# Kernel tuning notes

Measured on AMD Instinct MI355X. Metric: run time of the kernel, lower is better.

The kernel has to match this reference:

```python
import jax, jax.numpy as jnp
import numpy as np

N, C, E = 100000, 128, 600000
H = C // 2  # 64


def setup_inputs() -> dict:
    key = jax.random.key(0)
    k1, k2, k3, k4, k5, k6, k7, k8 = jax.random.split(key, 8)
    z_in = jax.random.normal(k1, (N, C), dtype=jnp.float32)
    z_out = jax.random.normal(k2, (N, C), dtype=jnp.float32)
    z_self = jax.random.normal(k3, (N, C), dtype=jnp.float32)
    edge_index = jax.random.randint(k4, (2, E), 0, N, dtype=jnp.int64)
    # MLP params: Linear(C, C//2) -> ELU -> (Dropout eval=no-op) -> Linear(C//2, 1)
    lim1 = 1.0 / np.sqrt(C)
    W1 = jax.random.uniform(k5, (C, H), minval=-lim1, maxval=lim1, dtype=jnp.float32)
    b1 = jax.random.uniform(k6, (H,), minval=-lim1, maxval=lim1, dtype=jnp.float32)
    lim2 = 1.0 / np.sqrt(H)
    W2 = jax.random.uniform(k7, (H, 1), minval=-lim2, maxval=lim2, dtype=jnp.float32)
    b2 = jax.random.uniform(k8, (1,), minval=-lim2, maxval=lim2, dtype=jnp.float32)
    return {"z_in": z_in, "z_out": z_out, "z_self": z_self,
            "edge_index": edge_index, "W1": W1, "b1": b1, "W2": W2, "b2": b2}


def reference(z_in, z_out, z_self, edge_index, W1, b1, W2, b2):
    v1 = z_out + z_self                       # [N, C]
    v2 = z_in + z_self                        # [N, C]
    value = v1[edge_index[0]] * v2[edge_index[1]]  # [E, C] gather + elementwise product
    h = jax.nn.elu(value @ W1 + b1)           # [E, H]; dropout is identity at eval
    logits = h @ W2 + b2                      # [E, 1]
    return jax.nn.sigmoid(logits)
```

## Files before the change

kernel.cpp:

```cpp
#include <hip/hip_runtime.h>
#include <hip/hip_bf16.h>

typedef __attribute__((ext_vector_type(8))) short short8;
typedef __attribute__((ext_vector_type(4))) float f32x4;

__device__ __forceinline__ unsigned short f2bf(float f) {
    unsigned u = __float_as_uint(f);
    u += 0x7fffu + ((u >> 16) & 1u);
    return (unsigned short)(u >> 16);
}

__device__ __forceinline__ unsigned pack_trunc(float lo, float hi) {
    return __builtin_amdgcn_perm(__float_as_uint(hi), __float_as_uint(lo), 0x07060302u);
}


__global__ __launch_bounds__(256) void prep_i8(
    const f32x4* __restrict__ zin, const f32x4* __restrict__ zout,
    const f32x4* __restrict__ zself,
    unsigned* __restrict__ q1, unsigned* __restrict__ q2,
    float* __restrict__ s1, float* __restrict__ s2, int N)
{
    const int lane = threadIdx.x & 63;
    const int wave = threadIdx.x >> 6;
    const int h    = lane >> 5;
    const int l32  = lane & 31;
    const int row  = blockIdx.x * 8 + wave * 2 + h;
    if (row >= N) return;
    const size_t rb = (size_t)row * 32 + l32;

    f32x4 o = __builtin_nontemporal_load(zout  + rb);
    f32x4 s = __builtin_nontemporal_load(zself + rb);
    f32x4 z = __builtin_nontemporal_load(zin   + rb);
    float v1[4] = {o.x + s.x, o.y + s.y, o.z + s.z, o.w + s.w};
    float v2[4] = {z.x + s.x, z.y + s.y, z.z + s.z, z.w + s.w};

    float m1 = fmaxf(fmaxf(fabsf(v1[0]), fabsf(v1[1])),
                     fmaxf(fabsf(v1[2]), fabsf(v1[3])));
    float m2 = fmaxf(fmaxf(fabsf(v2[0]), fabsf(v2[1])),
                     fmaxf(fabsf(v2[2]), fabsf(v2[3])));
#pragma unroll
    for (int off = 1; off < 32; off <<= 1) {
        m1 = fmaxf(m1, __shfl_xor(m1, off, 64));
        m2 = fmaxf(m2, __shfl_xor(m2, off, 64));
    }
    m1 = fmaxf(m1, 1e-20f);
    m2 = fmaxf(m2, 1e-20f);
    const float i1 = 127.0f / m1, i2 = 127.0f / m2;

    int qa[4], qb[4];
#pragma unroll
    for (int j = 0; j < 4; j++) {
        qa[j] = (int)rintf(v1[j] * i1);
        qb[j] = (int)rintf(v2[j] * i2);
    }
    unsigned wa = (unsigned)(qa[0] & 255) | ((unsigned)(qa[1] & 255) << 8) |
                  ((unsigned)(qa[2] & 255) << 16) | ((unsigned)qa[3] << 24);
    unsigned wb = (unsigned)(qb[0] & 255) | ((unsigned)(qb[1] & 255) << 8) |
                  ((unsigned)(qb[2] & 255) << 16) | ((unsigned)qb[3] << 24);
    q1[rb] = wa; q2[rb] = wb;
    if (l32 == 0) {
        s1[row] = m1 * (1.0f / 127.0f);
        s2[row] = m2 * (1.0f / 127.0f);
    }
}

__device__ __forceinline__ float pmul(unsigned aw, unsigned bw, int sh) {
    int a = (int)(signed char)(aw >> sh);
    int b = (int)(signed char)(bw >> sh);
    return (float)(a * b);
}

__global__ __launch_bounds__(256, 4) void edge_pipe_i8(
    const unsigned* __restrict__ q1, const unsigned* __restrict__ q2,
    const float* __restrict__ s1, const float* __restrict__ s2,
    const int* __restrict__ idx,
    const float* __restrict__ W1, const float* __restrict__ b1,
    const float* __restrict__ W2, const float* __restrict__ b2,
    float* __restrict__ out, int E, int ntiles)
{
    __shared__ __align__(16) unsigned short ldsW[16 * 64 * 8];

    const int tid  = threadIdx.x;
    const int wave = tid >> 6;
    const int lane = tid & 63;
    const int nn = lane & 15;
    const int q  = lane >> 4;

#pragma unroll
    for (int i = 0; i < 4; i++) {
        int p = tid * 4 + i;
        int f = p >> 6, l = p & 63;
        int kc = f >> 2, jt = f & 3, lq = (l >> 4) & 3, ln = l & 15;
        const float* wp = W1 + (size_t)(kc * 32 + lq * 8) * 64 + jt * 16 + ln;
        uint4 wv;
        wv.x = (unsigned)f2bf(wp[0 * 64]) | ((unsigned)f2bf(wp[1 * 64]) << 16);
        wv.y = (unsigned)f2bf(wp[2 * 64]) | ((unsigned)f2bf(wp[3 * 64]) << 16);
        wv.z = (unsigned)f2bf(wp[4 * 64]) | ((unsigned)f2bf(wp[5 * 64]) << 16);
        wv.w = (unsigned)f2bf(wp[6 * 64]) | ((unsigned)f2bf(wp[7 * 64]) << 16);
        *(uint4*)&ldsW[p * 8] = wv;
    }
    __syncthreads();

    float bias1[4], w2v[4];
#pragma unroll
    for (int jt = 0; jt < 4; jt++) {
        bias1[jt] = b1[jt * 16 + nn];
        w2v[jt]   = W2[jt * 16 + nn];
    }
    const float b2v = b2[0];

    const int nwaves = gridDim.x * 4;
    int tile = blockIdx.x * 4 + wave;
    if (tile >= ntiles) return;
    const int* __restrict__ idxE = idx + E;

    const int e0  = min(tile * 16 + nn, E - 1);
    const int t1  = tile + nwaves;
    const int tc1 = (t1 < ntiles) ? t1 : tile;
    const int e1  = min(tc1 * 16 + nn, E - 1);
    const int src0 = __builtin_nontemporal_load(idx  + e0);
    const int dst0 = __builtin_nontemporal_load(idxE + e0);
    int srcn = __builtin_nontemporal_load(idx  + e1);
    int dstn = __builtin_nontemporal_load(idxE + e1);

    float sN_a = s1[src0], sN_b = s2[dst0];

    uint2 a[4], b[4];
    {
        const uint2* p1 = (const uint2*)q1 + (size_t)src0 * 16;
        const uint2* p2 = (const uint2*)q2 + (size_t)dst0 * 16;
#pragma unroll
        for (int kc = 0; kc < 4; kc++) { a[kc] = p1[kc * 4 + q]; b[kc] = p2[kc * 4 + q]; }
    }

    for (; tile < ntiles; tile += nwaves) {
        const int t2  = tile + 2 * nwaves;
        const int tc2 = (t2 < ntiles) ? t2 : tile;
        const int e2  = min(tc2 * 16 + nn, E - 1);
        const int src2 = __builtin_nontemporal_load(idx  + e2);
        const int dst2 = __builtin_nontemporal_load(idxE + e2);

        const float s12 = sN_a * sN_b;
        short8 Af[4];
#pragma unroll
        for (int kc = 0; kc < 4; kc++) {
            uint4 p;
            p.x = pack_trunc(pmul(a[kc].x, b[kc].x,  0) * s12,
                             pmul(a[kc].x, b[kc].x,  8) * s12);
            p.y = pack_trunc(pmul(a[kc].x, b[kc].x, 16) * s12,
                             pmul(a[kc].x, b[kc].x, 24) * s12);
            p.z = pack_trunc(pmul(a[kc].y, b[kc].y,  0) * s12,
                             pmul(a[kc].y, b[kc].y,  8) * s12);
            p.w = pack_trunc(pmul(a[kc].y, b[kc].y, 16) * s12,
                             pmul(a[kc].y, b[kc].y, 24) * s12);
            Af[kc] = __builtin_bit_cast(short8, p);
        }

        {
            const uint2* p1 = (const uint2*)q1 + (size_t)srcn * 16;
            const uint2* p2 = (const uint2*)q2 + (size_t)dstn * 16;
#pragma unroll
            for (int kc = 0; kc < 4; kc++) { a[kc] = p1[kc * 4 + q]; b[kc] = p2[kc * 4 + q]; }
            sN_a = s1[srcn]; sN_b = s2[dstn];
        }
        srcn = src2; dstn = dst2;

        f32x4 acc[4];
#pragma unroll
        for (int jt = 0; jt < 4; jt++) acc[jt] = (f32x4){0.f, 0.f, 0.f, 0.f};
#pragma unroll
        for (int kc = 0; kc < 4; kc++) {
#pragma unroll
            for (int jt = 0; jt < 4; jt++) {
                short8 Bf = *(const short8*)&ldsW[((kc * 4 + jt) * 64 + lane) * 8];
                acc[jt] = __builtin_amdgcn_mfma_f32_16x16x32_bf16(Af[kc], Bf, acc[jt], 0, 0, 0);
            }
        }

        float ps[4];
#pragma unroll
        for (int r = 0; r < 4; r++) {
            float s = 0.f;
#pragma unroll
            for (int jt = 0; jt < 4; jt++) {
                float h = acc[jt][r] + bias1[jt];
                h = (h > 0.f) ? h : (__expf(h) - 1.f);
                s += h * w2v[jt];
            }
            ps[r] = s;
        }
#pragma unroll
        for (int off = 1; off < 16; off <<= 1) {
#pragma unroll
            for (int r = 0; r < 4; r++)
                ps[r] += __shfl_xor(ps[r], off, 64);
        }
        if (nn == 0) {
#pragma unroll
            for (int r = 0; r < 4; r++) {
                int e = tile * 16 + q * 4 + r;
                if (e < E) {
                    float x = ps[r] + b2v;
                    __builtin_nontemporal_store(1.f / (1.f + __expf(-x)), out + e);
                }
            }
        }
    }
}

__global__ __launch_bounds__(256) void edge_f32(
    const float* __restrict__ zin, const float* __restrict__ zout,
    const float* __restrict__ zself,
    const int* __restrict__ idx,
    const float* __restrict__ W1, const float* __restrict__ b1,
    const float* __restrict__ W2, const float* __restrict__ b2,
    float* __restrict__ out, int E, int ntiles)
{
    const int wave = threadIdx.x >> 6;
    const int lane = threadIdx.x & 63;
    const int nn = lane & 15;
    const int q  = lane >> 4;

    short8 Bf[4][4];
#pragma unroll
    for (int kc = 0; kc < 4; kc++)
#pragma unroll
        for (int jt = 0; jt < 4; jt++) {
            short8 v;
#pragma unroll
            for (int t = 0; t < 8; t++)
                v[t] = (short)f2bf(W1[(kc * 32 + q * 8 + t) * 64 + jt * 16 + nn]);
            Bf[kc][jt] = v;
        }
    float bias1[4], w2v[4];
#pragma unroll
    for (int jt = 0; jt < 4; jt++) {
        bias1[jt] = b1[jt * 16 + nn];
        w2v[jt]   = W2[jt * 16 + nn];
    }
    const float b2v = b2[0];

    const int nwaves = gridDim.x * 4;
    for (int tile = blockIdx.x * 4 + wave; tile < ntiles; tile += nwaves) {
        const int ebase = tile * 16;
        const int ee  = min(ebase + nn, E - 1);
        const int src = idx[ee];
        const int dst = idx[E + ee];

        short8 Af[4];
        const float* po  = zout  + (size_t)src * 128 + q * 8;
        const float* ps1 = zself + (size_t)src * 128 + q * 8;
        const float* pi  = zin   + (size_t)dst * 128 + q * 8;
        const float* ps2 = zself + (size_t)dst * 128 + q * 8;
#pragma unroll
        for (int kc = 0; kc < 4; kc++) {
            float4 oa = *(const float4*)(po  + kc * 32), ob = *(const float4*)(po  + kc * 32 + 4);
            float4 sa = *(const float4*)(ps1 + kc * 32), sb = *(const float4*)(ps1 + kc * 32 + 4);
            float4 ia = *(const float4*)(pi  + kc * 32), ib = *(const float4*)(pi  + kc * 32 + 4);
            float4 ta = *(const float4*)(ps2 + kc * 32), tb = *(const float4*)(ps2 + kc * 32 + 4);
            uint4 p;
            p.x = pack_trunc((oa.x + sa.x) * (ia.x + ta.x), (oa.y + sa.y) * (ia.y + ta.y));
            p.y = pack_trunc((oa.z + sa.z) * (ia.z + ta.z), (oa.w + sa.w) * (ia.w + ta.w));
            p.z = pack_trunc((ob.x + sb.x) * (ib.x + tb.x), (ob.y + sb.y) * (ib.y + tb.y));
            p.w = pack_trunc((ob.z + sb.z) * (ib.z + tb.z), (ob.w + sb.w) * (ib.w + tb.w));
            Af[kc] = __builtin_bit_cast(short8, p);
        }

        f32x4 acc[4];
#pragma unroll
        for (int jt = 0; jt < 4; jt++) acc[jt] = (f32x4){0.f, 0.f, 0.f, 0.f};
#pragma unroll
        for (int kc = 0; kc < 4; kc++)
#pragma unroll
            for (int jt = 0; jt < 4; jt++)
                acc[jt] = __builtin_amdgcn_mfma_f32_16x16x32_bf16(Af[kc], Bf[kc][jt], acc[jt], 0, 0, 0);

        float ps[4];
#pragma unroll
        for (int r = 0; r < 4; r++) {
            float s = 0.f;
#pragma unroll
            for (int jt = 0; jt < 4; jt++) {
                float h = acc[jt][r] + bias1[jt];
                h = (h > 0.f) ? h : (__expf(h) - 1.f);
                s += h * w2v[jt];
            }
            ps[r] = s;
        }
#pragma unroll
        for (int off = 1; off < 16; off <<= 1) {
#pragma unroll
            for (int r = 0; r < 4; r++)
                ps[r] += __shfl_xor(ps[r], off, 64);
        }
        if (nn == 0) {
#pragma unroll
            for (int r = 0; r < 4; r++) {
                int e = ebase + q * 4 + r;
                if (e < E) {
                    float x = ps[r] + b2v;
                    out[e] = 1.f / (1.f + __expf(-x));
                }
            }
        }
    }
}

extern "C" void kernel_launch(void* const* d_in, const int* in_sizes, int n_in,
                              void* d_out, int out_size, void* d_ws, size_t ws_size,
                              hipStream_t stream)
{
    const float* zin   = (const float*)d_in[0];
    const float* zout  = (const float*)d_in[1];
    const float* zself = (const float*)d_in[2];
    const int*   idx   = (const int*)d_in[3];
    const float* W1    = (const float*)d_in[4];
    const float* b1    = (const float*)d_in[5];
    const float* W2    = (const float*)d_in[6];
    const float* b2    = (const float*)d_in[7];
    float* out = (float*)d_out;

    const int NC = in_sizes[0];
    const int N  = NC / 128;
    const int E  = in_sizes[3] / 2;
    const int ntiles = (E + 15) / 16;
    const size_t need = (size_t)NC * 2 + (size_t)N * 8;

    if (ws_size >= need) {
        unsigned* q1 = (unsigned*)d_ws;
        unsigned* q2 = q1 + NC / 4;
        float* s1 = (float*)((char*)d_ws + (size_t)NC * 2);
        float* s2 = s1 + N;
        prep_i8<<<(N + 7) / 8, 256, 0, stream>>>(
            (const f32x4*)zin, (const f32x4*)zout, (const f32x4*)zself,
            q1, q2, s1, s2, N);

        const int cap = 2048;
        int iters = (ntiles + cap * 4 - 1) / (cap * 4);
        if (iters < 1) iters = 1;
        int eblocks = (ntiles + iters * 4 - 1) / (iters * 4);
        edge_pipe_i8<<<eblocks, 256, 0, stream>>>(
            q1, q2, s1, s2, idx, W1, b1, W2, b2, out, E, ntiles);
    } else {
        edge_f32<<<2048, 256, 0, stream>>>(
            zin, zout, zself, idx, W1, b1, W2, b2, out, E, ntiles);
    }
}
```

Baseline: 231.6 us.

## Permute int8 row layout for 16-byte loads and precompute per-edge scale products

The prep kernel now writes each quantized row in a permuted word order, so each lane fetches its four k-chunks with two 16-byte loads per row instead of four 8-byte loads. A new kernel precomputes the product of the source and destination scales for every edge into a workspace array, which the edge kernel streams with nontemporal loads and prefetches two tiles ahead. This removes the two dependent random scale gathers per edge from the main loop. The cost is an extra launch plus E*4 bytes of workspace traffic, and the fused path now requires a larger workspace.

```diff
diff --git a/kernel.cpp b/kernel.cpp
--- a/kernel.cpp
+++ b/kernel.cpp
@@ -58,10 +58,32 @@
                   ((unsigned)(qa[2] & 255) << 16) | ((unsigned)qa[3] << 24);
     unsigned wb = (unsigned)(qb[0] & 255) | ((unsigned)(qb[1] & 255) << 8) |
                   ((unsigned)(qb[2] & 255) << 16) | ((unsigned)qb[3] << 24);
-    q1[rb] = wa; q2[rb] = wb;
+    const int P = ((l32 >> 1) & 3) * 4 + (l32 & 1) + ((l32 >> 3) & 1) * 2 + (l32 & 16);
+    q1[(size_t)row * 32 + P] = wa;
+    q2[(size_t)row * 32 + P] = wb;
     if (l32 == 0) {
         s1[row] = m1 * (1.0f / 127.0f);
         s2[row] = m2 * (1.0f / 127.0f);
+    }
+}
+
+__global__ __launch_bounds__(256) void k_s12(
+    const int* __restrict__ idx, const float* __restrict__ s1,
+    const float* __restrict__ s2, float* __restrict__ e12, int E)
+{
+    int e = (blockIdx.x * 256 + threadIdx.x) * 4;
+    if (((E & 3) == 0) && e + 3 < E) {
+        int4 a = *(const int4*)(idx + e);
+        int4 b = *(const int4*)(idx + E + e);
+        float4 r;
+        r.x = s1[a.x] * s2[b.x];
+        r.y = s1[a.y] * s2[b.y];
+        r.z = s1[a.z] * s2[b.z];
+        r.w = s1[a.w] * s2[b.w];
+        *(float4*)(e12 + e) = r;
+    } else {
+        int hi = min(e + 4, E);
+        for (; e < hi; e++) e12[e] = s1[idx[e]] * s2[idx[E + e]];
     }
 }
 
@@ -71,9 +93,19 @@
     return (float)(a * b);
 }
 
+__device__ __forceinline__ short8 frag_i8(unsigned aw0, unsigned aw1,
+                                          unsigned bw0, unsigned bw1, float s12) {
+    uint4 p;
+    p.x = pack_trunc(pmul(aw0, bw0,  0) * s12, pmul(aw0, bw0,  8) * s12);
+    p.y = pack_trunc(pmul(aw0, bw0, 16) * s12, pmul(aw0, bw0, 24) * s12);
+    p.z = pack_trunc(pmul(aw1, bw1,  0) * s12, pmul(aw1, bw1,  8) * s12);
+    p.w = pack_trunc(pmul(aw1, bw1, 16) * s12, pmul(aw1, bw1, 24) * s12);
+    return __builtin_bit_cast(short8, p);
+}
+
 __global__ __launch_bounds__(256, 4) void edge_pipe_i8(
     const unsigned* __restrict__ q1, const unsigned* __restrict__ q2,
-    const float* __restrict__ s1, const float* __restrict__ s2,
+    const float* __restrict__ e12,
     const int* __restrict__ idx,
     const float* __restrict__ W1, const float* __restrict__ b1,
     const float* __restrict__ W2, const float* __restrict__ b2,
@@ -123,15 +155,15 @@
     const int dst0 = __builtin_nontemporal_load(idxE + e0);
     int srcn = __builtin_nontemporal_load(idx  + e1);
     int dstn = __builtin_nontemporal_load(idxE + e1);
-
-    float sN_a = s1[src0], sN_b = s2[dst0];
-
-    uint2 a[4], b[4];
+    float sc = __builtin_nontemporal_load(e12 + e0);
+    float sn = __builtin_nontemporal_load(e12 + e1);
+
+    uint4 a01, a23, b01, b23;
     {
-        const uint2* p1 = (const uint2*)q1 + (size_t)src0 * 16;
-        const uint2* p2 = (const uint2*)q2 + (size_t)dst0 * 16;
-#pragma unroll
-        for (int kc = 0; kc < 4; kc++) { a[kc] = p1[kc * 4 + q]; b[kc] = p2[kc * 4 + q]; }
+        const uint4* p1 = (const uint4*)q1 + (size_t)src0 * 8;
+        const uint4* p2 = (const uint4*)q2 + (size_t)dst0 * 8;
+        a01 = p1[q]; a23 = p1[4 + q];
+        b01 = p2[q]; b23 = p2[4 + q];
     }
 
     for (; tile < ntiles; tile += nwaves) {
@@ -140,30 +172,22 @@
         const int e2  = min(tc2 * 16 + nn, E - 1);
         const int src2 = __builtin_nontemporal_load(idx  + e2);
         const int dst2 = __builtin_nontemporal_load(idxE + e2);
-
-        const float s12 = sN_a * sN_b;
+        const float s2f = __builtin_nontemporal_load(e12 + e2);
+
+        const float s12 = sc;
         short8 Af[4];
-#pragma unroll
-        for (int kc = 0; kc < 4; kc++) {
-            uint4 p;
-            p.x = pack_trunc(pmul(a[kc].x, b[kc].x,  0) * s12,
-                             pmul(a[kc].x, b[kc].x,  8) * s12);
-            p.y = pack_trunc(pmul(a[kc].x, b[kc].x, 16) * s12,
-                             pmul(a[kc].x, b[kc].x, 24) * s12);
-            p.z = pack_trunc(pmul(a[kc].y, b[kc].y,  0) * s12,
-                             pmul(a[kc].y, b[kc].y,  8) * s12);
-            p.w = pack_trunc(pmul(a[kc].y, b[kc].y, 16) * s12,
-                             pmul(a[kc].y, b[kc].y, 24) * s12);
-            Af[kc] = __builtin_bit_cast(short8, p);
-        }
+        Af[0] = frag_i8(a01.x, a01.y, b01.x, b01.y, s12);
+        Af[1] = frag_i8(a01.z, a01.w, b01.z, b01.w, s12);
+        Af[2] = frag_i8(a23.x, a23.y, b23.x, b23.y, s12);
+        Af[3] = frag_i8(a23.z, a23.w, b23.z, b23.w, s12);
 
         {
-            const uint2* p1 = (const uint2*)q1 + (size_t)srcn * 16;
-            const uint2* p2 = (const uint2*)q2 + (size_t)dstn * 16;
-#pragma unroll
-            for (int kc = 0; kc < 4; kc++) { a[kc] = p1[kc * 4 + q]; b[kc] = p2[kc * 4 + q]; }
-            sN_a = s1[srcn]; sN_b = s2[dstn];
-        }
+            const uint4* p1 = (const uint4*)q1 + (size_t)srcn * 8;
+            const uint4* p2 = (const uint4*)q2 + (size_t)dstn * 8;
+            a01 = p1[q]; a23 = p1[4 + q];
+            b01 = p2[q]; b23 = p2[4 + q];
+        }
+        sc = sn; sn = s2f;
         srcn = src2; dstn = dst2;
 
         f32x4 acc[4];
@@ -325,23 +349,27 @@
     const int N  = NC / 128;
     const int E  = in_sizes[3] / 2;
     const int ntiles = (E + 15) / 16;
-    const size_t need = (size_t)NC * 2 + (size_t)N * 8;
+    const size_t off_s  = (size_t)NC * 2;
+    const size_t off_e  = off_s + (size_t)N * 8;
+    const size_t need   = off_e + (size_t)E * 4;
 
     if (ws_size >= need) {
         unsigned* q1 = (unsigned*)d_ws;
         unsigned* q2 = q1 + NC / 4;
-        float* s1 = (float*)((char*)d_ws + (size_t)NC * 2);
-        float* s2 = s1 + N;
+        float* s1  = (float*)((char*)d_ws + off_s);
+        float* s2  = s1 + N;
+        float* e12 = (float*)((char*)d_ws + off_e);
         prep_i8<<<(N + 7) / 8, 256, 0, stream>>>(
             (const f32x4*)zin, (const f32x4*)zout, (const f32x4*)zself,
             q1, q2, s1, s2, N);
+        k_s12<<<(E + 1023) / 1024, 256, 0, stream>>>(idx, s1, s2, e12, E);
 
         const int cap = 2048;
         int iters = (ntiles + cap * 4 - 1) / (cap * 4);
         if (iters < 1) iters = 1;
         int eblocks = (ntiles + iters * 4 - 1) / (iters * 4);
         edge_pipe_i8<<<eblocks, 256, 0, stream>>>(
-            q1, q2, s1, s2, idx, W1, b1, W2, b2, out, E, ntiles);
+            q1, q2, e12, idx, W1, b1, W2, b2, out, E, ntiles);
     } else {
         edge_f32<<<2048, 256, 0, stream>>>(
             zin, zout, zself, idx, W1, b1, W2, b2, out, E, ntiles);
```

After: 209.4 us. -9.6%, faster.
